# Kernel tuning notes

Measured on AMD Instinct MI355X. Metric: run time of the kernel, lower is better.

The kernel has to match this reference:

```python
import jax, jax.numpy as jnp
import numpy as np

S, C, E, G, H = 8192, 21, 128, 36, 1024  # seq_len, context_len, embed_dim, gazet_dim, hidden_dim
V_IN = 8000
T = 32              # tagset size incl. BOS/EOS
START, STOP = 30, 31
NEG = -10000.0


def setup_inputs() -> dict:
    key = jax.random.key(0)
    ks = jax.random.split(key, 10)
    contexts = jax.random.randint(ks[0], (S, C), 0, V_IN)
    gazet = jax.random.uniform(ks[1], (S, C, G), dtype=jnp.float32)
    train_labels = jax.random.randint(ks[2], (S,), 0, 30)  # base tags only
    emb = jax.random.normal(ks[3], (V_IN, E), dtype=jnp.float32) * 0.1
    D = C * (E + G)
    w1 = jax.random.normal(ks[4], (H, D), dtype=jnp.float32) / np.sqrt(D)
    b1 = jnp.zeros((H,), dtype=jnp.float32)
    w2 = jax.random.normal(ks[5], (T, H), dtype=jnp.float32) / np.sqrt(H)
    b2 = jnp.zeros((T,), dtype=jnp.float32)
    trans = jax.random.normal(ks[6], (T, T), dtype=jnp.float32)
    trans = trans.at[START, :].set(NEG)   # nothing transitions into START... (row = next tag)
    trans = trans.at[:, STOP].set(NEG)    # nothing leaves STOP (col = prev tag)
    return {"contexts": contexts, "gazet": gazet, "train_labels": train_labels,
            "emb": emb, "w1": w1, "b1": b1, "w2": w2, "b2": b2, "trans": trans}


def _feats(contexts, gazet, emb, w1, b1, w2, b2):
    x = jnp.concatenate([emb[contexts], gazet], axis=2)      # [S, C, E+G]
    x = x.reshape(x.shape[0], -1)                            # [S, C*(E+G)]
    h = jax.nn.relu(x @ w1.T + b1)                           # [S, H]  (dropout = identity in eval)
    return h @ w2.T + b2                                     # [S, T]


def _crf_forward(feats, trans):
    alpha0 = jnp.full((T,), NEG, dtype=feats.dtype).at[START].set(0.0)

    def step(alpha, feat):
        # scores[next, prev] = alpha[prev] + trans[next, prev] + feat[next]
        scores = alpha[None, :] + trans + feat[:, None]
        return jax.nn.logsumexp(scores, axis=1), None

    alpha, _ = jax.lax.scan(step, alpha0, feats)
    return jax.nn.logsumexp(alpha + trans[STOP])


def _gold_score(feats, tags, trans):
    tags_ext = jnp.concatenate([jnp.array([START], dtype=tags.dtype), tags])
    trans_sc = jnp.sum(trans[tags_ext[1:], tags_ext[:-1]])
    emit_sc = jnp.sum(feats[jnp.arange(feats.shape[0]), tags])
    return trans_sc + emit_sc + trans[STOP, tags[-1]]


def reference(contexts, gazet, train_labels, emb, w1, b1, w2, b2, trans):
    feats = _feats(contexts, gazet, emb, w1, b1, w2, b2)
    fwd = _crf_forward(feats, trans)
    gold = _gold_score(feats, train_labels, trans)
    return fwd - gold  # neg_log_likelihood (scalar)
```

## Files before the change

### kernel.cpp

```cpp
#include <hip/hip_runtime.h>

#define S_LEN 8192
#define C_CTX 21
#define E_DIM 128
#define G_DIM 36
#define H_DIM 1024
#define T_TAG 32
#define D_RAW 3444
#define DP 3456
#define GZP 768
#define START_TAG 30
#define STOP_TAG 31
#define NEGV -10000.0f
#define K_CHUNKS 64
#define L_CHUNK 128

typedef __bf16 bf16_t;
typedef __bf16 bf16x4 __attribute__((ext_vector_type(4)));
typedef __bf16 bf16x8 __attribute__((ext_vector_type(8)));
typedef float  f32x4  __attribute__((ext_vector_type(4)));

__device__ inline void async_copy16(const bf16_t* g, bf16_t* l) {
    __builtin_amdgcn_global_load_lds(
        (const __attribute__((address_space(1))) void*)g,
        (__attribute__((address_space(3))) void*)l, 16, 0, 0);
}

__global__ void build_all(const int* __restrict__ ctx, const float* __restrict__ gz,
                          const float* __restrict__ emb, const float* __restrict__ w1,
                          bf16_t* __restrict__ Xg, bf16_t* __restrict__ W,
                          bf16_t* __restrict__ EB) {
    const int b = blockIdx.x;
    if (b < 1024) {
        const int h = b;
        for (int g = threadIdx.x; g < DP / 4; g += 256) {
            bf16x4 o;
            if (g < 672) {
                const int knew = g * 4;
                const float4 v = *(const float4*)&w1[(size_t)h * D_RAW + (knew >> 7) * 164 + (knew & 127)];
                o = bf16x4{(bf16_t)v.x, (bf16_t)v.y, (bf16_t)v.z, (bf16_t)v.w};
            } else {
                const int m = g * 4 - 2688;
                float t[4];
#pragma unroll
                for (int u = 0; u < 4; ++u) {
                    const int mm = m + u;
                    t[u] = (mm < 756) ? w1[(size_t)h * D_RAW + (mm / 36) * 164 + 128 + (mm % 36)] : 0.f;
                }
                o = bf16x4{(bf16_t)t[0], (bf16_t)t[1], (bf16_t)t[2], (bf16_t)t[3]};
            }
            *(bf16x4*)&W[(size_t)h * DP + g * 4] = o;
        }
    } else if (b < 3072) {
        const int s_base = (b - 1024) * 4;
        for (int g = threadIdx.x; g < 4 * 192; g += 256) {
            const int r = g / 192, gg = g - r * 192;
            const int s = s_base + r;
            bf16x4 o = bf16x4{(bf16_t)0.f, (bf16_t)0.f, (bf16_t)0.f, (bf16_t)0.f};
            if (gg < 189) {
                const float4 v = *(const float4*)&gz[(size_t)s * 756 + gg * 4];
                o = bf16x4{(bf16_t)v.x, (bf16_t)v.y, (bf16_t)v.z, (bf16_t)v.w};
            }
            *(bf16x4*)&Xg[(size_t)s * GZP + gg * 4] = o;
        }
    } else {
        const size_t base = (size_t)(b - 3072) * 2048;
        for (int g = threadIdx.x; g < 512; g += 256) {
            const float4 v = *(const float4*)&emb[base + g * 4];
            bf16x4 o = bf16x4{(bf16_t)v.x, (bf16_t)v.y, (bf16_t)v.z, (bf16_t)v.w};
            *(bf16x4*)&EB[base + g * 4] = o;
        }
    }
}

__global__ __launch_bounds__(256) void gemm1(const int* __restrict__ ctx,
                                             const bf16_t* __restrict__ EB,
                                             const bf16_t* __restrict__ Xg,
                                             const bf16_t* __restrict__ W,
                                             const float* __restrict__ b1,
                                             const float* __restrict__ w2,
                                             const float* __restrict__ b2,
                                             float* __restrict__ Fp) {
    __shared__ bf16_t As[2][128 * 64];
    __shared__ bf16_t Bs[2][128 * 64];
    __shared__ unsigned short ctxs[128 * 21];
    const int tid  = threadIdx.x;
    const int wave = tid >> 6, lane = tid & 63;
    const int s0 = blockIdx.x * 128, h0 = blockIdx.y * 128;
    const int wm = (wave >> 1) * 64;
    const int wn = (wave & 1) * 64;

    const int arow = tid >> 3;
    const int akg  = (tid & 7) ^ (arow & 7);
    const bf16_t* gB = W + (size_t)(h0 + arow) * DP + akg * 8;

    const int lrow  = lane & 15;
    const int khalf = lane >> 4;
    const int lr7   = lrow & 7;

    for (int j = tid; j < 128 * C_CTX; j += 256)
        ctxs[j] = (unsigned short)ctx[s0 * C_CTX + j];
    asm volatile("s_waitcnt lgkmcnt(0)" ::: "memory");
    __builtin_amdgcn_s_barrier();

    {
        const int e0 = akg * 8;
#pragma unroll
        for (int i = 0; i < 4; ++i) {
            const int cv = ctxs[(i * 32 + arow) * 21];
            async_copy16(EB + (size_t)cv * 128 + e0, &As[0][(i * 256 + tid) * 8]);
        }
#pragma unroll
        for (int i = 0; i < 4; ++i)
            async_copy16(gB + (size_t)i * 32 * DP, &Bs[0][(i * 256 + tid) * 8]);
    }
    asm volatile("s_waitcnt vmcnt(0)" ::: "memory");
    __builtin_amdgcn_s_barrier();

    f32x4 acc[4][4] = {};
    const int NT = DP / 64;
    for (int t = 0; t < NT; ++t) {
        const int cur = t & 1, nxt = cur ^ 1;
        const int tt = t + 1;
        const bool st = tt < NT;

        bf16x8 a[2][2][2];
        bf16x8 b[2][2][2];
#pragma unroll
        for (int ks = 0; ks < 2; ++ks) {
            const int kgr = ((ks * 4 + khalf) ^ lr7) * 8;
#pragma unroll
            for (int sp = 0; sp < 2; ++sp)
#pragma unroll
                for (int mt = 0; mt < 2; ++mt)
                    a[sp][ks][mt] = *(const bf16x8*)&As[cur][(wm + sp * 32 + mt * 16 + lrow) * 64 + kgr];
#pragma unroll
            for (int qn = 0; qn < 2; ++qn)
#pragma unroll
                for (int nt = 0; nt < 2; ++nt)
                    b[qn][ks][nt] = *(const bf16x8*)&Bs[cur][(wn + qn * 32 + nt * 16 + lrow) * 64 + kgr];
        }
        if (st) {
            if (tt < 42) {
                const int c_ = tt >> 1;
                const int e0 = (tt & 1) * 64 + akg * 8;
#pragma unroll
                for (int i = 0; i < 4; ++i) {
                    const int cv = ctxs[(i * 32 + arow) * 21 + c_];
                    async_copy16(EB + (size_t)cv * 128 + e0, &As[nxt][(i * 256 + tid) * 8]);
                }
            } else {
                const int m0 = (tt - 42) * 64 + akg * 8;
#pragma unroll
                for (int i = 0; i < 4; ++i)
                    async_copy16(Xg + (size_t)(s0 + i * 32 + arow) * GZP + m0, &As[nxt][(i * 256 + tid) * 8]);
            }
#pragma unroll
            for (int i = 0; i < 4; ++i)
                async_copy16(gB + (size_t)i * 32 * DP + tt * 64, &Bs[nxt][(i * 256 + tid) * 8]);
        }
        __builtin_amdgcn_s_setprio(1);
#pragma unroll
        for (int ks = 0; ks < 2; ++ks)
#pragma unroll
            for (int sp = 0; sp < 2; ++sp)
#pragma unroll
                for (int qn = 0; qn < 2; ++qn)
#pragma unroll
                    for (int mt = 0; mt < 2; ++mt)
#pragma unroll
                        for (int nt = 0; nt < 2; ++nt)
                            acc[sp * 2 + mt][qn * 2 + nt] = __builtin_amdgcn_mfma_f32_16x16x32_bf16(
                                a[sp][ks][mt], b[qn][ks][nt], acc[sp * 2 + mt][qn * 2 + nt], 0, 0, 0);
        __builtin_amdgcn_s_setprio(0);
        if (st) asm volatile("s_waitcnt vmcnt(0)" ::: "memory");
        __builtin_amdgcn_s_barrier();
    }

    bf16_t* Hl = &As[0][0];
    bf16_t* Wl = &Bs[0][0];

#pragma unroll
    for (int rep = 0; rep < 2; ++rep) {
        const int t8 = tid >> 3;
        const int hl = (tid & 7) * 2 + rep;
        const float* wsrc = w2 + (size_t)t8 * H_DIM + h0 + hl * 8;
        const float4 y0 = *(const float4*)wsrc;
        const float4 y1 = *(const float4*)(wsrc + 4);
        bf16x8 wv = {(bf16_t)y0.x, (bf16_t)y0.y, (bf16_t)y0.z, (bf16_t)y0.w,
                     (bf16_t)y1.x, (bf16_t)y1.y, (bf16_t)y1.z, (bf16_t)y1.w};
        *(bf16x8*)&Wl[(t8 * 16 + (hl ^ (t8 & 7))) * 8] = wv;
    }

    const int crow = (lane >> 4) * 4;
    const int ccol = lane & 15;
#pragma unroll
    for (int nt = 0; nt < 4; ++nt) {
        const int jl = wn + nt * 16 + ccol;
        const float bv = b1[h0 + jl];
#pragma unroll
        for (int mt = 0; mt < 4; ++mt) {
#pragma unroll
            for (int r = 0; r < 4; ++r) {
                const int sl = wm + mt * 16 + crow + r;
                const float v = acc[mt][nt][r] + bv;
                Hl[sl * 128 + ((jl >> 3) ^ (sl & 7)) * 8 + (jl & 7)] = (bf16_t)fmaxf(v, 0.f);
            }
        }
    }
    __syncthreads();

    f32x4 acc2[2][2] = {};
    const int wm2 = wave * 32;
#pragma unroll
    for (int ks = 0; ks < 4; ++ks) {
        const int slot = ((ks * 4 + khalf) ^ lr7) * 8;
        bf16x8 ah[2], bw[2];
#pragma unroll
        for (int mt = 0; mt < 2; ++mt)
            ah[mt] = *(const bf16x8*)&Hl[(wm2 + mt * 16 + lrow) * 128 + slot];
#pragma unroll
        for (int nt = 0; nt < 2; ++nt)
            bw[nt] = *(const bf16x8*)&Wl[(nt * 16 + lrow) * 128 + slot];
#pragma unroll
        for (int mt = 0; mt < 2; ++mt)
#pragma unroll
            for (int nt = 0; nt < 2; ++nt)
                acc2[mt][nt] = __builtin_amdgcn_mfma_f32_16x16x32_bf16(ah[mt], bw[nt], acc2[mt][nt], 0, 0, 0);
    }
    const int bj = h0 >> 7;
#pragma unroll
    for (int nt = 0; nt < 2; ++nt) {
        const int tcol = nt * 16 + ccol;
        const float badd = (bj == 7) ? b2[tcol] : 0.f;
#pragma unroll
        for (int mt = 0; mt < 2; ++mt) {
#pragma unroll
            for (int r = 0; r < 4; ++r) {
                const int sr = s0 + wm2 + mt * 16 + crow + r;
                Fp[((size_t)bj * S_LEN + sr) * T_TAG + tcol] = acc2[mt][nt][r] + badd;
            }
        }
    }
}

__global__ __launch_bounds__(512) void crfA(const float* __restrict__ Fp,
                                            const float* __restrict__ trans,
                                            float* __restrict__ QT,
                                            float* __restrict__ sigma,
                                            const int* __restrict__ lab,
                                            float* __restrict__ gold_part) {
    __shared__ float fl[L_CHUNK * 32];
    __shared__ float vb[8][64];
    __shared__ float wred[8];
    const int c    = blockIdx.x >> 2;
    const int tid  = threadIdx.x;
    const int wave = tid >> 6;
    const int lane = tid & 63;
    const int n    = lane & 31;
    const int h    = lane >> 5;
    const int p    = ((blockIdx.x & 3) << 3) + wave;
    const int s0   = c * L_CHUNK;
    for (int i = tid; i < L_CHUNK * 32; i += 512) {
        const size_t idx = (size_t)s0 * 32 + i;
        float accf = 0.f;
#pragma unroll
        for (int j = 0; j < 8; ++j) accf += Fp[(size_t)j * S_LEN * T_TAG + idx];
        fl[i] = accf;
    }
    __syncthreads();

    const bool goldblk = (blockIdx.x & 3) == 0;
    float gterm = 0.f;
    if (goldblk && tid < L_CHUNK) {
        const int s  = s0 + tid;
        const int tg = lab[s];
        const int tp = (s == 0) ? START_TAG : lab[s - 1];
        gterm = fl[tid * 32 + tg] + trans[tg * T_TAG + tp];
    }
#pragma unroll
    for (int off = 32; off; off >>= 1) gterm += __shfl_down(gterm, off, 64);
    if (goldblk && lane == 0) wred[wave] = gterm;
    __syncthreads();
    if (goldblk && tid == 0) {
        float gsum = 0.f;
#pragma unroll
        for (int i = 0; i < 8; ++i) gsum += wred[i];
        gold_part[c] = gsum;
    }

    float etl[16];
#pragma unroll
    for (int j = 0; j < 16; ++j) etl[j] = __expf(trans[n * 32 + h * 16 + j]);

    float* vrow = &vb[wave][0];
    float v  = __expf(trans[n * 32 + p] + fl[n]);
    float sg = 0.f;
    for (int s = 1; s < L_CHUNK; ++s) {
        vrow[lane] = v;
        __builtin_amdgcn_s_waitcnt(0xC07F);
        float a0 = 0.f, a1 = 0.f, a2 = 0.f, a3 = 0.f;
#pragma unroll
        for (int q = 0; q < 4; ++q) {
            const float4 wv = *(const float4*)&vrow[h * 16 + q * 4];
            a0 = __builtin_fmaf(etl[q * 4 + 0], wv.x, a0);
            a1 = __builtin_fmaf(etl[q * 4 + 1], wv.y, a1);
            a2 = __builtin_fmaf(etl[q * 4 + 2], wv.z, a2);
            a3 = __builtin_fmaf(etl[q * 4 + 3], wv.w, a3);
        }
        float part = (a0 + a1) + (a2 + a3);
        part += __shfl_xor(part, 32);
        v = __expf(fl[s * 32 + n]) * part;
        if ((s & 7) == 7) {
            float m = v;
#pragma unroll
            for (int off = 16; off; off >>= 1) m = fmaxf(m, __shfl_xor(m, off, 32));
            if (m > 0.f) { v *= 1.0f / m; sg += __logf(m); }
        }
    }
    if (h == 0) {
        QT[(c * 32 + p) * 32 + n] = v;
        if (n == 0) sigma[c * 32 + p] = sg;
    }
}

__global__ __launch_bounds__(1024) void crf_fold(const float* __restrict__ Qin,
                                                 const float* __restrict__ Sin,
                                                 const int fold, const int final,
                                                 float* __restrict__ Qout,
                                                 float* __restrict__ Sout,
                                                 const float* __restrict__ trans,
                                                 const float* __restrict__ gold_part,
                                                 const int* __restrict__ lab,
                                                 float* __restrict__ out) {
    __shared__ float A[32][33];
    __shared__ float M[32][33];
    __shared__ float sgf[32];
    __shared__ float gold_s;

    const int t = threadIdx.x;
    const int p = t >> 5, n = t & 31;
    const int c0 = blockIdx.x * fold;

    if (final && t == 0) {
        float s = 0.f;
#pragma unroll
        for (int i = 0; i < K_CHUNKS; ++i) s += gold_part[i];
        gold_s = s + trans[STOP_TAG * T_TAG + lab[S_LEN - 1]];
    }

    A[n][p] = Qin[(size_t)(c0 * 32 + p) * 32 + n];
    float sA = Sin[c0 * 32 + p];
    float mreg = Qin[(size_t)((c0 + 1) * 32 + p) * 32 + n];

    for (int i = 1; i < fold; ++i) {
        const float sMn = Sin[(c0 + i) * 32 + n];
        float mmax = sMn;
#pragma unroll
        for (int off = 16; off; off >>= 1) mmax = fmaxf(mmax, __shfl_xor(mmax, off, 32));
        const float sMp = Sin[(c0 + i) * 32 + p];
        __syncthreads();
        M[n][p] = mreg * __expf(sMp - mmax);
        if (i + 1 < fold) mreg = Qin[(size_t)((c0 + i + 1) * 32 + p) * 32 + n];
        __syncthreads();
        float acc = 0.f;
#pragma unroll 8
        for (int k = 0; k < 32; ++k)
            acc += M[n][k] * A[k][p];
        float cm = acc;
#pragma unroll
        for (int off = 16; off; off >>= 1) cm = fmaxf(cm, __shfl_xor(cm, off, 32));
        cm = fmaxf(cm, 1e-37f);
        __syncthreads();
        A[n][p] = acc / cm;
        sA = sA + mmax + __logf(cm);
    }
    __syncthreads();

    if (!final) {
        Qout[(size_t)(blockIdx.x * 32 + p) * 32 + n] = A[n][p];
        if (n == 0) Sout[blockIdx.x * 32 + p] = sA;
        return;
    }

    if (n == 0) sgf[p] = sA;
    __syncthreads();
    if (t < 32) {
        float v = A[t][START_TAG] * __expf(trans[STOP_TAG * T_TAG + t]);
#pragma unroll
        for (int off = 16; off; off >>= 1) v += __shfl_xor(v, off, 32);
        if (t == 0) out[0] = sgf[START_TAG] + __logf(v) - gold_s;
    }
}

extern "C" void kernel_launch(void* const* d_in, const int* in_sizes, int n_in,
                              void* d_out, int out_size, void* d_ws, size_t ws_size,
                              hipStream_t stream) {
    const int*   ctx   = (const int*)d_in[0];
    const float* gz    = (const float*)d_in[1];
    const int*   lab   = (const int*)d_in[2];
    const float* emb   = (const float*)d_in[3];
    const float* w1    = (const float*)d_in[4];
    const float* b1    = (const float*)d_in[5];
    const float* w2    = (const float*)d_in[6];
    const float* b2    = (const float*)d_in[7];
    const float* trans = (const float*)d_in[8];
    float* out = (float*)d_out;

    char* ws = (char*)d_ws;
    bf16_t* W1b = (bf16_t*)(ws + 0);
    bf16_t* EB  = (bf16_t*)(ws + 7077888);
    bf16_t* Xg  = (bf16_t*)(ws + 9126400);
    float*  Fp  = (float*)(ws + 21709312);
    float*  goldp = (float*)(ws + 30097920);
    float*  QT  = (float*)(ws + 31146496);
    float*  sg  = (float*)(ws + 31408640);
    float*  Q1  = (float*)(ws + 31416832);
    float*  S1  = (float*)(ws + 31449600);

    build_all<<<3572, 256, 0, stream>>>(ctx, gz, emb, w1, Xg, W1b, EB);
    gemm1<<<dim3(S_LEN / 128, H_DIM / 128), 256, 0, stream>>>(ctx, EB, Xg, W1b, b1, w2, b2, Fp);
    crfA<<<K_CHUNKS * 4, 512, 0, stream>>>(Fp, trans, QT, sg, lab, goldp);
    crf_fold<<<8, 1024, 0, stream>>>(QT, sg, 8, 0, Q1, S1, trans, nullptr, nullptr, nullptr);
    crf_fold<<<1, 1024, 0, stream>>>(Q1, S1, 8, 1, nullptr, nullptr, trans, goldp, lab, out);
}
```

Baseline: 219.0 us.

## Use eight waves per gemm1 block with 64x32 warp tiles

Doubles gemm1 workgroup size from 256 to 512 threads while keeping the 128x128 block tile, so each wave computes a 64x32 sub-tile instead of 64x64. Async global-to-LDS loads, the w2 staging and the second small GEMM epilogue are redistributed across the eight waves. This is meant to raise latency hiding and cut per-wave accumulator registers, at the cost of more LDS reads per MFMA (less register reuse of A fragments) and more barrier participants.

```diff
diff --git a/kernel.cpp b/kernel.cpp
--- a/kernel.cpp
+++ b/kernel.cpp
@@ -73,7 +73,7 @@
     }
 }
 
-__global__ __launch_bounds__(256) void gemm1(const int* __restrict__ ctx,
+__global__ __launch_bounds__(512) void gemm1(const int* __restrict__ ctx,
                                              const bf16_t* __restrict__ EB,
                                              const bf16_t* __restrict__ Xg,
                                              const bf16_t* __restrict__ W,
@@ -87,8 +87,8 @@
     const int tid  = threadIdx.x;
     const int wave = tid >> 6, lane = tid & 63;
     const int s0 = blockIdx.x * 128, h0 = blockIdx.y * 128;
-    const int wm = (wave >> 1) * 64;
-    const int wn = (wave & 1) * 64;
+    const int wm = (wave >> 2) * 64;
+    const int wn = (wave & 3) * 32;
 
     const int arow = tid >> 3;
     const int akg  = (tid & 7) ^ (arow & 7);
@@ -98,7 +98,7 @@
     const int khalf = lane >> 4;
     const int lr7   = lrow & 7;
 
-    for (int j = tid; j < 128 * C_CTX; j += 256)
+    for (int j = tid; j < 128 * C_CTX; j += 512)
         ctxs[j] = (unsigned short)ctx[s0 * C_CTX + j];
     asm volatile("s_waitcnt lgkmcnt(0)" ::: "memory");
     __builtin_amdgcn_s_barrier();
@@ -106,72 +106,64 @@
     {
         const int e0 = akg * 8;
 #pragma unroll
-        for (int i = 0; i < 4; ++i) {
-            const int cv = ctxs[(i * 32 + arow) * 21];
-            async_copy16(EB + (size_t)cv * 128 + e0, &As[0][(i * 256 + tid) * 8]);
-        }
-#pragma unroll
-        for (int i = 0; i < 4; ++i)
-            async_copy16(gB + (size_t)i * 32 * DP, &Bs[0][(i * 256 + tid) * 8]);
+        for (int i = 0; i < 2; ++i) {
+            const int cv = ctxs[(i * 64 + arow) * 21];
+            async_copy16(EB + (size_t)cv * 128 + e0, &As[0][(i * 512 + tid) * 8]);
+        }
+#pragma unroll
+        for (int i = 0; i < 2; ++i)
+            async_copy16(gB + (size_t)i * 64 * DP, &Bs[0][(i * 512 + tid) * 8]);
     }
     asm volatile("s_waitcnt vmcnt(0)" ::: "memory");
     __builtin_amdgcn_s_barrier();
 
-    f32x4 acc[4][4] = {};
+    f32x4 acc[4][2] = {};
     const int NT = DP / 64;
     for (int t = 0; t < NT; ++t) {
         const int cur = t & 1, nxt = cur ^ 1;
         const int tt = t + 1;
         const bool st = tt < NT;
 
-        bf16x8 a[2][2][2];
-        bf16x8 b[2][2][2];
+        bf16x8 a[2][4];
+        bf16x8 b[2][2];
 #pragma unroll
         for (int ks = 0; ks < 2; ++ks) {
             const int kgr = ((ks * 4 + khalf) ^ lr7) * 8;
 #pragma unroll
-            for (int sp = 0; sp < 2; ++sp)
-#pragma unroll
-                for (int mt = 0; mt < 2; ++mt)
-                    a[sp][ks][mt] = *(const bf16x8*)&As[cur][(wm + sp * 32 + mt * 16 + lrow) * 64 + kgr];
-#pragma unroll
-            for (int qn = 0; qn < 2; ++qn)
-#pragma unroll
-                for (int nt = 0; nt < 2; ++nt)
-                    b[qn][ks][nt] = *(const bf16x8*)&Bs[cur][(wn + qn * 32 + nt * 16 + lrow) * 64 + kgr];
+            for (int mt = 0; mt < 4; ++mt)
+                a[ks][mt] = *(const bf16x8*)&As[cur][(wm + mt * 16 + lrow) * 64 + kgr];
+#pragma unroll
+            for (int nt = 0; nt < 2; ++nt)
+                b[ks][nt] = *(const bf16x8*)&Bs[cur][(wn + nt * 16 + lrow) * 64 + kgr];
         }
         if (st) {
             if (tt < 42) {
                 const int c_ = tt >> 1;
                 const int e0 = (tt & 1) * 64 + akg * 8;
 #pragma unroll
-                for (int i = 0; i < 4; ++i) {
-                    const int cv = ctxs[(i * 32 + arow) * 21 + c_];
-                    async_copy16(EB + (size_t)cv * 128 + e0, &As[nxt][(i * 256 + tid) * 8]);
+                for (int i = 0; i < 2; ++i) {
+                    const int cv = ctxs[(i * 64 + arow) * 21 + c_];
+                    async_copy16(EB + (size_t)cv * 128 + e0, &As[nxt][(i * 512 + tid) * 8]);
                 }
             } else {
                 const int m0 = (tt - 42) * 64 + akg * 8;
 #pragma unroll
-                for (int i = 0; i < 4; ++i)
-                    async_copy16(Xg + (size_t)(s0 + i * 32 + arow) * GZP + m0, &As[nxt][(i * 256 + tid) * 8]);
+                for (int i = 0; i < 2; ++i)
+                    async_copy16(Xg + (size_t)(s0 + i * 64 + arow) * GZP + m0, &As[nxt][(i * 512 + tid) * 8]);
             }
 #pragma unroll
-            for (int i = 0; i < 4; ++i)
-                async_copy16(gB + (size_t)i * 32 * DP + tt * 64, &Bs[nxt][(i * 256 + tid) * 8]);
+            for (int i = 0; i < 2; ++i)
+                async_copy16(gB + (size_t)i * 64 * DP + tt * 64, &Bs[nxt][(i * 512 + tid) * 8]);
         }
         __builtin_amdgcn_s_setprio(1);
 #pragma unroll
         for (int ks = 0; ks < 2; ++ks)
 #pragma unroll
-            for (int sp = 0; sp < 2; ++sp)
-#pragma unroll
-                for (int qn = 0; qn < 2; ++qn)
-#pragma unroll
-                    for (int mt = 0; mt < 2; ++mt)
-#pragma unroll
-                        for (int nt = 0; nt < 2; ++nt)
-                            acc[sp * 2 + mt][qn * 2 + nt] = __builtin_amdgcn_mfma_f32_16x16x32_bf16(
-                                a[sp][ks][mt], b[qn][ks][nt], acc[sp * 2 + mt][qn * 2 + nt], 0, 0, 0);
+            for (int mt = 0; mt < 4; ++mt)
+#pragma unroll
+                for (int nt = 0; nt < 2; ++nt)
+                    acc[mt][nt] = __builtin_amdgcn_mfma_f32_16x16x32_bf16(
+                        a[ks][mt], b[ks][nt], acc[mt][nt], 0, 0, 0);
         __builtin_amdgcn_s_setprio(0);
         if (st) asm volatile("s_waitcnt vmcnt(0)" ::: "memory");
         __builtin_amdgcn_s_barrier();
@@ -180,10 +172,9 @@
     bf16_t* Hl = &As[0][0];
     bf16_t* Wl = &Bs[0][0];
 
-#pragma unroll
-    for (int rep = 0; rep < 2; ++rep) {
-        const int t8 = tid >> 3;
-        const int hl = (tid & 7) * 2 + rep;
+    {
+        const int t8 = tid >> 4;
+        const int hl = tid & 15;
         const float* wsrc = w2 + (size_t)t8 * H_DIM + h0 + hl * 8;
         const float4 y0 = *(const float4*)wsrc;
         const float4 y1 = *(const float4*)(wsrc + 4);
@@ -195,7 +186,7 @@
     const int crow = (lane >> 4) * 4;
     const int ccol = lane & 15;
 #pragma unroll
-    for (int nt = 0; nt < 4; ++nt) {
+    for (int nt = 0; nt < 2; ++nt) {
         const int jl = wn + nt * 16 + ccol;
         const float bv = b1[h0 + jl];
 #pragma unroll
@@ -210,23 +201,19 @@
     }
     __syncthreads();
 
-    f32x4 acc2[2][2] = {};
-    const int wm2 = wave * 32;
+    f32x4 acc2[2] = {};
+    const int wm2 = wave * 16;
 #pragma unroll
     for (int ks = 0; ks < 4; ++ks) {
         const int slot = ((ks * 4 + khalf) ^ lr7) * 8;
-        bf16x8 ah[2], bw[2];
-#pragma unroll
-        for (int mt = 0; mt < 2; ++mt)
-            ah[mt] = *(const bf16x8*)&Hl[(wm2 + mt * 16 + lrow) * 128 + slot];
+        bf16x8 ah = *(const bf16x8*)&Hl[(wm2 + lrow) * 128 + slot];
+        bf16x8 bw[2];
 #pragma unroll
         for (int nt = 0; nt < 2; ++nt)
             bw[nt] = *(const bf16x8*)&Wl[(nt * 16 + lrow) * 128 + slot];
 #pragma unroll
-        for (int mt = 0; mt < 2; ++mt)
-#pragma unroll
-            for (int nt = 0; nt < 2; ++nt)
-                acc2[mt][nt] = __builtin_amdgcn_mfma_f32_16x16x32_bf16(ah[mt], bw[nt], acc2[mt][nt], 0, 0, 0);
+        for (int nt = 0; nt < 2; ++nt)
+            acc2[nt] = __builtin_amdgcn_mfma_f32_16x16x32_bf16(ah, bw[nt], acc2[nt], 0, 0, 0);
     }
     const int bj = h0 >> 7;
 #pragma unroll
@@ -234,12 +221,9 @@
         const int tcol = nt * 16 + ccol;
         const float badd = (bj == 7) ? b2[tcol] : 0.f;
 #pragma unroll
-        for (int mt = 0; mt < 2; ++mt) {
-#pragma unroll
-            for (int r = 0; r < 4; ++r) {
-                const int sr = s0 + wm2 + mt * 16 + crow + r;
-                Fp[((size_t)bj * S_LEN + sr) * T_TAG + tcol] = acc2[mt][nt][r] + badd;
-            }
+        for (int r = 0; r < 4; ++r) {
+            const int sr = s0 + wm2 + crow + r;
+            Fp[((size_t)bj * S_LEN + sr) * T_TAG + tcol] = acc2[nt][r] + badd;
         }
     }
 }
@@ -419,7 +403,7 @@
     float*  S1  = (float*)(ws + 31449600);
 
     build_all<<<3572, 256, 0, stream>>>(ctx, gz, emb, w1, Xg, W1b, EB);
-    gemm1<<<dim3(S_LEN / 128, H_DIM / 128), 256, 0, stream>>>(ctx, EB, Xg, W1b, b1, w2, b2, Fp);
+    gemm1<<<dim3(S_LEN / 128, H_DIM / 128), 512, 0, stream>>>(ctx, EB, Xg, W1b, b1, w2, b2, Fp);
     crfA<<<K_CHUNKS * 4, 512, 0, stream>>>(Fp, trans, QT, sg, lab, goldp);
     crf_fold<<<8, 1024, 0, stream>>>(QT, sg, 8, 0, Q1, S1, trans, nullptr, nullptr, nullptr);
     crf_fold<<<1, 1024, 0, stream>>>(Q1, S1, 8, 1, nullptr, nullptr, trans, goldp, lab, out);
```

New measurement: 223.5 us. +2.0%, slower.
